# Performance work log

Hardware: AMD Instinct MI355X
Metric: run time of the kernel (lower is better)

The kernel has to match this reference:

```python
import jax, jax.numpy as jnp
import numpy as np

M, N, K, C, H = 100000, 8192, 32, 256, 8
DH = C // H
FF = 512
R = (15, 15, 7)  # 2*MAXRANGE-1 per axis for MAXRANGE=[8,8,4]


def _layer_norm(x, g, b, eps=1e-5):
    mu = jnp.mean(x, axis=-1, keepdims=True)
    xc = x - mu
    var = jnp.mean(xc * xc, axis=-1, keepdims=True)
    return xc * jax.lax.rsqrt(var + eps) * g + b


def setup_inputs() -> dict:
    key = jax.random.key(0)
    ks = iter(jax.random.split(key, 40))
    d = {}
    d['voxel_features'] = jax.random.normal(next(ks), (M, C), jnp.float32)
    d['query_coords'] = jax.random.normal(next(ks), (N, 3), jnp.float32)
    d['query_indices'] = jax.random.randint(next(ks), (N,), 0, M)
    d['gather_indices'] = jax.random.randint(next(ks), (N, K), 0, M)
    d['gather_mask'] = jax.random.randint(next(ks), (N, K), 0, 2).astype(bool)
    d['rel_x'] = jax.random.randint(next(ks), (N, K), 0, R[0])
    d['rel_y'] = jax.random.randint(next(ks), (N, K), 0, R[1])
    d['rel_z'] = jax.random.randint(next(ks), (N, K), 0, R[2])
    s = 0.02
    # pos_proj: Conv1d(3, C, 1) == linear on coords
    d['w_pos'] = jax.random.normal(next(ks), (3, C), jnp.float32) * s
    d['b_pos'] = jnp.zeros((C,), jnp.float32)
    for nm in ['q', 'k', 'v', 'proj']:
        d['w_' + nm] = jax.random.normal(next(ks), (C, C), jnp.float32) * (C ** -0.5)
        d['b_' + nm] = jnp.zeros((C,), jnp.float32)
    d['ln1_g'] = jnp.ones((C,), jnp.float32); d['ln1_b'] = jnp.zeros((C,), jnp.float32)
    d['ln2_g'] = jnp.ones((C,), jnp.float32); d['ln2_b'] = jnp.zeros((C,), jnp.float32)
    d['w_ff1'] = jax.random.normal(next(ks), (C, FF), jnp.float32) * (C ** -0.5)
    d['b_ff1'] = jnp.zeros((FF,), jnp.float32)
    d['w_ff2'] = jax.random.normal(next(ks), (FF, C), jnp.float32) * (FF ** -0.5)
    d['b_ff2'] = jnp.zeros((C,), jnp.float32)
    # per-axis relative position tables: [H, DH, 2W-1] for q-side and k-side
    for m in ['q', 'k']:
        for ax, r in zip(['x', 'y', 'z'], R):
            d[f'pos_{m}{ax}'] = jax.random.normal(next(ks), (H, DH, r), jnp.float32) * s
    return d


def reference(voxel_features, query_coords, query_indices, gather_indices, gather_mask,
              rel_x, rel_y, rel_z,
              w_pos, b_pos, w_q, b_q, w_k, b_k, w_v, b_v, w_proj, b_proj,
              ln1_g, ln1_b, ln2_g, ln2_b, w_ff1, b_ff1, w_ff2, b_ff2,
              pos_qx, pos_qy, pos_qz, pos_kx, pos_ky, pos_kz):
    x = _layer_norm(voxel_features, ln1_g, ln1_b)           # [M, C] pre-norm
    # gather window centers (queries) + positional projection of coords
    q_in = x[query_indices] + jax.nn.relu(query_coords @ w_pos + b_pos)  # [N, C]
    kv_in = x[gather_indices]                                # [N, K, C]
    kv_in = jnp.where(gather_mask[..., None], 0.0, kv_in)
    q = (q_in @ w_q + b_q).reshape(N, H, DH)
    k = (kv_in @ w_k + b_k).reshape(N, K, H, DH)
    v = (kv_in @ w_v + b_v).reshape(N, K, H, DH)
    logits = jnp.einsum('nhd,nkhd->nhk', q, k) * (DH ** -0.5)  # [N, H, K]
    # query-side per-axis relative position bias: contract q with table, gather at rel idx
    for pos, rel in ((pos_qx, rel_x), (pos_qy, rel_y), (pos_qz, rel_z)):
        qp = jnp.einsum('nhd,hdr->nhr', q, pos)              # [N, H, R]
        logits = logits + jnp.take_along_axis(qp, rel[:, None, :], axis=2)
    # key-side per-axis relative position bias
    for pos, rel in ((pos_kx, rel_x), (pos_ky, rel_y), (pos_kz, rel_z)):
        kp = jnp.einsum('nkhd,hdr->nkhr', k, pos)            # [N, K, H, R]
        bias = jnp.take_along_axis(kp, rel[:, :, None, None], axis=3)[..., 0]  # [N, K, H]
        logits = logits + bias.transpose(0, 2, 1)
    logits = jnp.where(gather_mask[:, None, :], -1e9, logits)
    attn = jax.nn.softmax(logits, axis=-1)
    out = jnp.einsum('nhk,nkhd->nhd', attn, v).reshape(N, C) @ w_proj + b_proj
    act = voxel_features[query_indices] + out                # residual (pre-norm block)
    h = jax.nn.relu(_layer_norm(act, ln2_g, ln2_b) @ w_ff1 + b_ff1) @ w_ff2 + b_ff2
    return act + h                                           # [N, C]
```

## Files before the change

kernel.cpp:

```cpp
#include <hip/hip_runtime.h>
#include <hip/hip_bf16.h>
#include <math.h>

#define MV   100000
#define NQ   8192
#define KN   32
#define CH   256
#define NH   8
#define DHD  32
#define FFD  512
#define NG   (NQ*KN)
#define QPW  37
#define QPN  (NH*QPW)
#define QPL  320
#define ASTR 40

typedef __bf16 bf16x8 __attribute__((ext_vector_type(8)));
typedef float  f32x4  __attribute__((ext_vector_type(4)));

__device__ __forceinline__ float bf2f(unsigned short u) {
    return __uint_as_float(((unsigned int)u) << 16);
}
__device__ __forceinline__ unsigned short f2bf(float f) {
    unsigned int x = __float_as_uint(f);
    unsigned int r = x + 0x7FFFu + ((x >> 16) & 1u);
    return (unsigned short)(r >> 16);
}
__device__ __forceinline__ void glds16(const unsigned short* g, unsigned short* l) {
    __builtin_amdgcn_global_load_lds(
        (const __attribute__((address_space(1))) void*)g,
        (__attribute__((address_space(3))) void*)l, 16, 0, 0);
}

__global__ __launch_bounds__(256) void k_detect_mask(const unsigned char* __restrict__ raw,
                                                     int* __restrict__ flags) {
    __shared__ int any;
    if (threadIdx.x == 0) any = 0;
    __syncthreads();
    const uint4* p = (const uint4*)raw;
    int i = blockIdx.x * 256 + threadIdx.x;
    uint4 v = p[i];
    if ((v.x | v.y | v.z | v.w) & 0xFFFFFF00u) any = 1;
    __syncthreads();
    if (threadIdx.x == 0) flags[blockIdx.x] = any;
}

__global__ __launch_bounds__(256) void k_prep(const float* __restrict__ w_k,
                                              const float* __restrict__ w_v,
                                              const float* __restrict__ w_ff1,
                                              const float* __restrict__ w_ff2,
                                              const float* __restrict__ w_proj,
                                              const float* __restrict__ w_q,
                                              const float* __restrict__ b_k,
                                              const float* __restrict__ b_v,
                                              const float* __restrict__ pos_qx,
                                              const float* __restrict__ pos_qy,
                                              const float* __restrict__ pos_qz,
                                              const void* __restrict__ mask_raw,
                                              const int* __restrict__ gidx,
                                              const int* __restrict__ flags,
                                              unsigned short* __restrict__ w_kv_t,
                                              unsigned short* __restrict__ w1_t,
                                              unsigned short* __restrict__ w2_t,
                                              unsigned short* __restrict__ wp_t,
                                              unsigned short* __restrict__ wq_t,
                                              unsigned short* __restrict__ wqp_t,
                                              float* __restrict__ bkv,
                                              float* __restrict__ zbias,
                                              int* __restrict__ mask_i,
                                              unsigned char* __restrict__ touched) {
    __shared__ int bl;
    if (threadIdx.x == 0) {
        int a = 0;
        #pragma unroll 8
        for (int i = 0; i < 64; i++) a |= flags[i];
        bl = a;
    }
    __syncthreads();
    int byteLayout = bl;
    int idx = blockIdx.x * 256 + threadIdx.x;
    if (blockIdx.x == 0 && threadIdx.x < 512)
        bkv[threadIdx.x] = (threadIdx.x < 256) ? b_k[threadIdx.x]
                                               : b_v[threadIdx.x - 256];
    if (idx < QPL) zbias[idx] = 0.f;
    if (idx < NG) {
        int mv = byteLayout ? (int)((const unsigned char*)mask_raw)[idx]
                            : ((const int*)mask_raw)[idx];
        mask_i[idx] = (mv != 0) ? 1 : 0;
        if (mv == 0) touched[gidx[idx]] = 1;
    }
    if (idx < 512 * 256) {
        int col = idx >> 8, j = idx & 255;
        float v = (col < 256) ? w_k[j * 256 + col] : w_v[j * 256 + (col - 256)];
        w_kv_t[idx] = f2bf(v);
    }
    if (idx < 512 * 256) {
        int n = idx >> 8, k = idx & 255;
        w1_t[idx] = f2bf(w_ff1[k * FFD + n]);
    }
    if (idx < 256 * 512) {
        int n = idx >> 9, k = idx & 511;
        w2_t[idx] = f2bf(w_ff2[k * CH + n]);
    }
    if (idx < 256 * 256) {
        int n = idx >> 8, k = idx & 255;
        wp_t[idx] = f2bf(w_proj[k * CH + n]);
        wq_t[idx] = f2bf(w_q[k * CH + n]);
    }
    if (idx < QPL * 256) {
        int col = idx >> 8, k = idx & 255;
        float v = 0.f;
        if (col < QPN) {
            int h = col / QPW, r = col % QPW;
            int h2 = k >> 5, d = k & 31;
            if (h2 == h) {
                if (r < 15)      v = pos_qx[(h * DHD + d) * 15 + r];
                else if (r < 30) v = pos_qy[(h * DHD + d) * 15 + (r - 15)];
                else             v = pos_qz[(h * DHD + d) * 7  + (r - 30)];
            }
        }
        wqp_t[idx] = f2bf(v);
    }
}

__global__ __launch_bounds__(256) void k_posc(const float* __restrict__ pos_kx,
                                              const float* __restrict__ pos_ky,
                                              const float* __restrict__ pos_kz,
                                              float* __restrict__ comb) {
    int idx = blockIdx.x * 256 + threadIdx.x;
    if (idx >= 8 * 15 * 15 * 7 * 32) return;
    int d = idx & 31, r = idx >> 5;
    int rz = r % 7;  r /= 7;
    int ry = r % 15; r /= 15;
    int rx = r % 15; int h = r / 15;
    comb[idx] = pos_kx[(h * DHD + d) * 15 + rx]
              + pos_ky[(h * DHD + d) * 15 + ry]
              + pos_kz[(h * DHD + d) * 7  + rz];
}

__global__ __launch_bounds__(256) void k_ln(const float* __restrict__ x,
                                            const float* __restrict__ g,
                                            const float* __restrict__ b,
                                            unsigned short* __restrict__ o,
                                            int nrows) {
    int wid = threadIdx.x >> 6, lane = threadIdx.x & 63;
    int row = blockIdx.x * 4 + wid;
    if (row >= nrows) return;
    const float4 v = *(const float4*)(x + (size_t)row * CH + lane * 4);
    float s  = v.x + v.y + v.z + v.w;
    float sq = v.x * v.x + v.y * v.y + v.z * v.z + v.w * v.w;
    #pragma unroll
    for (int off = 1; off < 64; off <<= 1) {
        s  += __shfl_xor(s,  off);
        sq += __shfl_xor(sq, off);
    }
    float mu  = s * (1.f / CH);
    float var = sq * (1.f / CH) - mu * mu;
    float rs  = rsqrtf(var + 1e-5f);
    float4 gv = *(const float4*)(g + lane * 4);
    float4 bv = *(const float4*)(b + lane * 4);
    ushort4 ov;
    ov.x = f2bf((v.x - mu) * rs * gv.x + bv.x);
    ov.y = f2bf((v.y - mu) * rs * gv.y + bv.y);
    ov.z = f2bf((v.z - mu) * rs * gv.z + bv.z);
    ov.w = f2bf((v.w - mu) * rs * gv.w + bv.w);
    *(ushort4*)(o + (size_t)row * CH + lane * 4) = ov;
}

__global__ __launch_bounds__(256) void k_qin(const unsigned short* __restrict__ ln_x,
                                             const float* __restrict__ coords,
                                             const int* __restrict__ qidx,
                                             const float* __restrict__ w_pos,
                                             const float* __restrict__ b_pos,
                                             unsigned short* __restrict__ qin) {
    int c = threadIdx.x;
    int nb = blockIdx.x * 8;
    float wp0 = w_pos[c], wp1 = w_pos[CH + c], wp2 = w_pos[2 * CH + c], bp = b_pos[c];
    #pragma unroll
    for (int qq = 0; qq < 8; qq++) {
        int n = nb + qq;
        float p = bp + coords[n * 3] * wp0 + coords[n * 3 + 1] * wp1 + coords[n * 3 + 2] * wp2;
        p = fmaxf(p, 0.f);
        int qi = qidx[n];
        qin[(size_t)n * CH + c] = f2bf(bf2f(ln_x[(size_t)qi * CH + c]) + p);
    }
}

__global__ __launch_bounds__(256) void k_kv(const unsigned short* __restrict__ ln_x,
                                            const unsigned short* __restrict__ w_kv_t,
                                            const float* __restrict__ bkv,
                                            const unsigned char* __restrict__ touched,
                                            unsigned short* __restrict__ kv) {
    __shared__ __align__(16) unsigned short As[8 * 4096];
    __shared__ __align__(16) unsigned short Bs[4096];
    const int tid = threadIdx.x;
    const int w = tid >> 6, l = tid & 63;
    const int wr = w >> 1, wc = w & 1;
    const int rowbase = blockIdx.x * 128;
    const int sr = l >> 2, sq = l & 3;
    const int ml = l & 15, qd = l >> 4;

    int ra0 = rowbase + w * 16 + sr;
    int ra1 = rowbase + 64 + w * 16 + sr;
    int ok0 = (ra0 < MV) && touched[ra0 < MV ? ra0 : 0];
    int ok1 = (ra1 < MV) && touched[ra1 < MV ? ra1 : 0];
    const unsigned short* pa0 = ln_x + (size_t)(ok0 ? ra0 : rowbase) * CH + sq * 8;
    const unsigned short* pa1 = ln_x + (size_t)(ok1 ? ra1 : rowbase) * CH + sq * 8;
    unsigned short* lA0 = As + w * 512;
    unsigned short* lA1 = As + 2048 + w * 512;
    unsigned short* lB0 = Bs + w * 512;
    unsigned short* lB1 = Bs + 2048 + w * 512;

    #pragma unroll
    for (int c = 0; c < 8; c++) {
        glds16(pa0 + c * 32, lA0 + c * 4096);
        glds16(pa1 + c * 32, lA1 + c * 4096);
    }

    for (int ct = 0; ct < 4; ct++) {
        const int col0 = ct * 128;
        const unsigned short* pb0 = w_kv_t + (size_t)(col0 + w * 16 + sr) * CH + sq * 8;
        const unsigned short* pb1 = w_kv_t + (size_t)(col0 + 64 + w * 16 + sr) * CH + sq * 8;
        f32x4 acc[4][4];
        #pragma unroll
        for (int mt = 0; mt < 4; mt++)
            #pragma unroll
            for (int nt = 0; nt < 4; nt++)
                acc[mt][nt] = (f32x4){0.f, 0.f, 0.f, 0.f};

        for (int c = 0; c < 8; c++) {
            __syncthreads();
            glds16(pb0 + c * 32, lB0);
            glds16(pb1 + c * 32, lB1);
            __syncthreads();
            bf16x8 af[4], bf[4];
            const unsigned short* Ac = As + c * 4096;
            #pragma unroll
            for (int mt = 0; mt < 4; mt++)
                af[mt] = *(const bf16x8*)(Ac + (wr * 64 + mt * 16 + ml) * 32 + qd * 8);
            #pragma unroll
            for (int nt = 0; nt < 4; nt++)
                bf[nt] = *(const bf16x8*)(Bs + (wc * 64 + nt * 16 + ml) * 32 + qd * 8);
            #pragma unroll
            for (int mt = 0; mt < 4; mt++)
                #pragma unroll
                for (int nt = 0; nt < 4; nt++)
                    acc[mt][nt] = __builtin_amdgcn_mfma_f32_16x16x32_bf16(af[mt], bf[nt], acc[mt][nt], 0, 0, 0);
        }

        float bb[4];
        #pragma unroll
        for (int nt = 0; nt < 4; nt++)
            bb[nt] = bkv[col0 + wc * 64 + nt * 16 + ml];
        #pragma unroll
        for (int mt = 0; mt < 4; mt++) {
            __syncthreads();
            #pragma unroll
            for (int nt = 0; nt < 4; nt++) {
                int lcol = wc * 64 + nt * 16 + ml;
                #pragma unroll
                for (int i = 0; i < 4; i++)
                    Bs[wr * 2048 + (qd * 4 + i) * 128 + lcol] = f2bf(acc[mt][nt][i] + bb[nt]);
            }
            __syncthreads();
            int rl = tid >> 4, cc = (tid & 15) * 8;
            int g0 = rowbase + mt * 16 + rl;
            int g1 = rowbase + 64 + mt * 16 + rl;
            if (g0 < MV && touched[g0])
                *(uint4*)(kv + (size_t)g0 * 512 + col0 + cc) = *(const uint4*)(Bs + rl * 128 + cc);
            if (g1 < MV && touched[g1])
                *(uint4*)(kv + (size_t)g1 * 512 + col0 + cc) = *(const uint4*)(Bs + 2048 + rl * 128 + cc);
        }
    }
}

template <int KD, int EPI, int LDO>
__global__ __launch_bounds__(256) void k_mm(const unsigned short* __restrict__ A,
                                            const unsigned short* __restrict__ Bt_g,
                                            const float* __restrict__ bias,
                                            const float* __restrict__ res,
                                            const int* __restrict__ qidx,
                                            unsigned short* __restrict__ out_bf,
                                            float* __restrict__ out_f) {
    __shared__ __align__(16) unsigned short As[128 * ASTR];
    __shared__ __align__(16) unsigned short Bs[64 * ASTR];
    int tid = threadIdx.x;
    int w = tid >> 6, l = tid & 63;
    int rowbase = blockIdx.y * 128;
    int col0 = blockIdx.x * 64;
    int r0 = tid >> 2, qt = tid & 3;
    const unsigned short* a0p = A + (size_t)(rowbase + r0) * KD + qt * 8;
    const unsigned short* a1p = A + (size_t)(rowbase + 64 + r0) * KD + qt * 8;

    f32x4 acc[2][4];
    #pragma unroll
    for (int mt = 0; mt < 2; mt++)
        #pragma unroll
        for (int nt = 0; nt < 4; nt++)
            acc[mt][nt] = (f32x4){0.f, 0.f, 0.f, 0.f};

    const int ml = l & 15, qd = l >> 4;
    for (int kk = 0; kk < KD; kk += 32) {
        __syncthreads();
        uint4 v0 = *(const uint4*)(a0p + kk);
        uint4 v1 = *(const uint4*)(a1p + kk);
        *(uint4*)(As + r0 * ASTR + qt * 8)        = v0;
        *(uint4*)(As + (64 + r0) * ASTR + qt * 8) = v1;
        {
            uint4 bv = *(const uint4*)(Bt_g + (size_t)(col0 + r0) * KD + kk + qt * 8);
            *(uint4*)(Bs + r0 * ASTR + qt * 8) = bv;
        }
        __syncthreads();
        bf16x8 a0 = *(const bf16x8*)(As + (w * 32 + ml) * ASTR + qd * 8);
        bf16x8 a1 = *(const bf16x8*)(As + (w * 32 + 16 + ml) * ASTR + qd * 8);
        #pragma unroll
        for (int nt = 0; nt < 4; nt++) {
            bf16x8 bb = *(const bf16x8*)(Bs + (nt * 16 + ml) * ASTR + qd * 8);
            acc[0][nt] = __builtin_amdgcn_mfma_f32_16x16x32_bf16(a0, bb, acc[0][nt], 0, 0, 0);
            acc[1][nt] = __builtin_amdgcn_mfma_f32_16x16x32_bf16(a1, bb, acc[1][nt], 0, 0, 0);
        }
    }

    #pragma unroll
    for (int nt = 0; nt < 4; nt++) {
        int col = col0 + nt * 16 + ml;
        float bv = bias[col];
        #pragma unroll
        for (int mt = 0; mt < 2; mt++) {
            int rl = w * 32 + mt * 16 + qd * 4;
            #pragma unroll
            for (int i = 0; i < 4; i++) {
                int row = rowbase + rl + i;
                float v = acc[mt][nt][i] + bv;
                if (EPI == 0) {
                    out_bf[(size_t)row * LDO + col] = f2bf(fmaxf(v, 0.f));
                } else if (EPI == 1) {
                    out_f[(size_t)row * CH + col] = v + res[(size_t)row * CH + col];
                } else if (EPI == 2) {
                    int qi = qidx[row];
                    out_f[(size_t)row * CH + col] = v + res[(size_t)qi * CH + col];
                } else if (EPI == 3) {
                    out_f[(size_t)row * CH + col] = v;
                    out_bf[(size_t)row * CH + col] = f2bf(v);
                } else {
                    out_f[(size_t)row * LDO + col] = v;
                }
            }
        }
    }
}

__global__ __launch_bounds__(256) void k_attn2(const float* __restrict__ qbuf,
                                               const float* __restrict__ qp,
                                               const unsigned short* __restrict__ kvmat,
                                               const int* __restrict__ gidx,
                                               const int* __restrict__ mask_i,
                                               const int* __restrict__ rel_x,
                                               const int* __restrict__ rel_y,
                                               const int* __restrict__ rel_z,
                                               const float* __restrict__ comb,
                                               const float* __restrict__ b_v,
                                               unsigned short* __restrict__ attnln) {
    __shared__ float q_s[1024];
    __shared__ float qp_s[4 * QPL];
    __shared__ float attn_s[4 * 256];
    __shared__ int mask_s[4 * 32];
    int tid = threadIdx.x;
    int qb = blockIdx.x * 4;
    for (int i = tid; i < 1024; i += 256) q_s[i] = qbuf[(size_t)qb * CH + i];
    for (int i = tid; i < 4 * QPL; i += 256) qp_s[i] = qp[(size_t)qb * QPL + i];
    if (tid < 128) mask_s[tid] = mask_i[qb * 32 + tid];
    __syncthreads();
    int h = tid >> 5, k = tid & 31;
    const float scale = 0.17677669529663687f;
    for (int qq = 0; qq < 4; qq++) {
        int n = qb + qq;
        int gi = n * KN + k;
        int mk = mask_s[qq * 32 + k];
        float lg = -1e9f;
        if (!mk) {
            int rx = rel_x[gi], ry = rel_y[gi], rz = rel_z[gi];
            int g = gidx[gi];
            const uint4* kp = (const uint4*)(kvmat + (size_t)g * 512 + h * DHD);
            float kv[32];
            #pragma unroll
            for (int j = 0; j < 4; j++) {
                uint4 u = kp[j];
                kv[j * 8 + 0] = bf2f((unsigned short)(u.x & 0xFFFF));
                kv[j * 8 + 1] = bf2f((unsigned short)(u.x >> 16));
                kv[j * 8 + 2] = bf2f((unsigned short)(u.y & 0xFFFF));
                kv[j * 8 + 3] = bf2f((unsigned short)(u.y >> 16));
                kv[j * 8 + 4] = bf2f((unsigned short)(u.z & 0xFFFF));
                kv[j * 8 + 5] = bf2f((unsigned short)(u.z >> 16));
                kv[j * 8 + 6] = bf2f((unsigned short)(u.w & 0xFFFF));
                kv[j * 8 + 7] = bf2f((unsigned short)(u.w >> 16));
            }
            const float* cp = comb + ((((h * 15 + rx) * 15 + ry) * 7 + rz) << 5);
            float s1 = 0.f, s2 = 0.f;
            const float* qrow = q_s + qq * CH + h * DHD;
            #pragma unroll
            for (int d = 0; d < 32; d++) {
                s1 += kv[d] * qrow[d];
                s2 += kv[d] * cp[d];
            }
            lg = s1 * scale + s2
               + qp_s[qq * QPL + h * QPW + rx]
               + qp_s[qq * QPL + h * QPW + 15 + ry]
               + qp_s[qq * QPL + h * QPW + 30 + rz];
        }
        float mx = lg;
        #pragma unroll
        for (int off = 1; off <= 16; off <<= 1) mx = fmaxf(mx, __shfl_xor(mx, off));
        float e = mk ? 0.f : __expf(lg - mx);
        float sm = e;
        #pragma unroll
        for (int off = 1; off <= 16; off <<= 1) sm += __shfl_xor(sm, off);
        attn_s[qq * 256 + tid] = (sm > 0.f) ? e / sm : 0.f;
    }
    __syncthreads();

    int w = tid >> 6, l = tid & 63;
    int n = qb + w;
    int hh = l >> 3;
    float a0 = 0.f, a1 = 0.f, a2 = 0.f, a3 = 0.f;
    int nm = 0;
    for (int kk = 0; kk < KN; kk++) {
        if (mask_s[w * 32 + kk]) continue;
        nm++;
        int g = gidx[n * 32 + kk];
        ushort4 v4 = *(const ushort4*)(kvmat + (size_t)g * 512 + 256 + l * 4);
        float av = attn_s[w * 256 + hh * 32 + kk];
        a0 += av * bf2f(v4.x);
        a1 += av * bf2f(v4.y);
        a2 += av * bf2f(v4.z);
        a3 += av * bf2f(v4.w);
    }
    int col = l * 4;
    if (nm == 0) {
        a0 = b_v[col]; a1 = b_v[col + 1]; a2 = b_v[col + 2]; a3 = b_v[col + 3];
    }
    ushort4 o;
    o.x = f2bf(a0); o.y = f2bf(a1); o.z = f2bf(a2); o.w = f2bf(a3);
    *(ushort4*)(attnln + (size_t)n * CH + col) = o;
}

extern "C" void kernel_launch(void* const* d_in, const int* in_sizes, int n_in,
                              void* d_out, int out_size, void* d_ws, size_t ws_size,
                              hipStream_t stream) {
    (void)in_sizes; (void)n_in; (void)out_size; (void)ws_size;
    const float* vox    = (const float*)d_in[0];
    const float* coords = (const float*)d_in[1];
    const int*   qidx   = (const int*)d_in[2];
    const int*   gidx   = (const int*)d_in[3];
    const void*  mraw   = d_in[4];
    const int*   rel_x  = (const int*)d_in[5];
    const int*   rel_y  = (const int*)d_in[6];
    const int*   rel_z  = (const int*)d_in[7];
    const float* w_pos  = (const float*)d_in[8];
    const float* b_pos  = (const float*)d_in[9];
    const float* w_q    = (const float*)d_in[10];
    const float* b_q    = (const float*)d_in[11];
    const float* w_k    = (const float*)d_in[12];
    const float* b_k    = (const float*)d_in[13];
    const float* w_v    = (const float*)d_in[14];
    const float* b_v    = (const float*)d_in[15];
    const float* w_proj = (const float*)d_in[16];
    const float* b_proj = (const float*)d_in[17];
    const float* ln1_g  = (const float*)d_in[18];
    const float* ln1_b  = (const float*)d_in[19];
    const float* ln2_g  = (const float*)d_in[20];
    const float* ln2_b  = (const float*)d_in[21];
    const float* w_ff1  = (const float*)d_in[22];
    const float* b_ff1  = (const float*)d_in[23];
    const float* w_ff2  = (const float*)d_in[24];
    const float* b_ff2  = (const float*)d_in[25];
    const float* pos_qx = (const float*)d_in[26];
    const float* pos_qy = (const float*)d_in[27];
    const float* pos_qz = (const float*)d_in[28];
    const float* pos_kx = (const float*)d_in[29];
    const float* pos_ky = (const float*)d_in[30];
    const float* pos_kz = (const float*)d_in[31];

    char* p = (char*)d_ws;
    auto take = [&](size_t n) { char* r = p; p += (n + 255) & ~(size_t)255; return r; };
    unsigned short* ln_x    = (unsigned short*)take((size_t)MV * CH * 2);
    unsigned short* w_kv_t  = (unsigned short*)take((size_t)512 * 256 * 2);
    unsigned short* w1_t    = (unsigned short*)take((size_t)512 * 256 * 2);
    unsigned short* w2_t    = (unsigned short*)take((size_t)256 * 512 * 2);
    unsigned short* wp_t    = (unsigned short*)take((size_t)256 * 256 * 2);
    unsigned short* wq_t    = (unsigned short*)take((size_t)256 * 256 * 2);
    unsigned short* wqp_t   = (unsigned short*)take((size_t)QPL * 256 * 2);
    float*          bkv     = (float*)take(512 * 4);
    float*          zbias   = (float*)take(QPL * 4);
    int*            flags   = (int*)take(64 * 4);
    int*            mask_i  = (int*)take((size_t)NG * 4);
    unsigned char*  touched = (unsigned char*)take(MV);
    float*          comb    = (float*)take((size_t)8 * 15 * 15 * 7 * 32 * 4);
    unsigned short* qin     = (unsigned short*)take((size_t)NQ * CH * 2);
    float*          qbuf    = (float*)take((size_t)NQ * CH * 4);
    unsigned short* qbf     = (unsigned short*)take((size_t)NQ * CH * 2);
    float*          qp      = (float*)take((size_t)NQ * QPL * 4);
    unsigned short* kvmat   = (unsigned short*)take((size_t)MV * 512 * 2);
    unsigned short* attnln  = (unsigned short*)take((size_t)NQ * CH * 2);
    float*          actbuf  = (float*)take((size_t)NQ * CH * 4);
    unsigned short* actln   = (unsigned short*)take((size_t)NQ * CH * 2);
    unsigned short* hbuf    = (unsigned short*)take((size_t)NQ * FFD * 2);

    hipMemsetAsync(touched, 0, MV, stream);
    hipLaunchKernelGGL(k_detect_mask, dim3(64), dim3(256), 0, stream,
                       (const unsigned char*)mraw, flags);
    hipLaunchKernelGGL(k_prep, dim3(NG / 256), dim3(256), 0, stream,
                       w_k, w_v, w_ff1, w_ff2, w_proj, w_q, b_k, b_v,
                       pos_qx, pos_qy, pos_qz, mraw, gidx, flags,
                       w_kv_t, w1_t, w2_t, wp_t, wq_t, wqp_t, bkv, zbias,
                       mask_i, touched);
    hipLaunchKernelGGL(k_posc, dim3((8 * 15 * 15 * 7 * 32 + 255) / 256), dim3(256), 0, stream,
                       pos_kx, pos_ky, pos_kz, comb);
    hipLaunchKernelGGL(k_ln, dim3(MV / 4 + 1), dim3(256), 0, stream,
                       vox, ln1_g, ln1_b, ln_x, MV);
    hipLaunchKernelGGL(k_qin, dim3(NQ / 8), dim3(256), 0, stream,
                       ln_x, coords, qidx, w_pos, b_pos, qin);
    hipLaunchKernelGGL(k_kv, dim3((MV + 127) / 128), dim3(256), 0, stream,
                       ln_x, w_kv_t, bkv, touched, kvmat);
    hipLaunchKernelGGL(HIP_KERNEL_NAME(k_mm<256, 3, CH>), dim3(4, NQ / 128), dim3(256), 0, stream,
                       qin, wq_t, b_q, (const float*)nullptr, (const int*)nullptr,
                       qbf, qbuf);
    hipLaunchKernelGGL(HIP_KERNEL_NAME(k_mm<256, 4, QPL>), dim3(QPL / 64, NQ / 128), dim3(256), 0, stream,
                       qbf, wqp_t, zbias, (const float*)nullptr, (const int*)nullptr,
                       (unsigned short*)nullptr, qp);
    hipLaunchKernelGGL(k_attn2, dim3(NQ / 4), dim3(256), 0, stream,
                       qbuf, qp, kvmat, gidx, mask_i, rel_x, rel_y, rel_z,
                       comb, b_v, attnln);
    hipLaunchKernelGGL(HIP_KERNEL_NAME(k_mm<256, 2, CH>), dim3(4, NQ / 128), dim3(256), 0, stream,
                       attnln, wp_t, b_proj, vox, qidx,
                       (unsigned short*)nullptr, actbuf);
    hipLaunchKernelGGL(k_ln, dim3(NQ / 4), dim3(256), 0, stream,
                       actbuf, ln2_g, ln2_b, actln, NQ);
    hipLaunchKernelGGL(HIP_KERNEL_NAME(k_mm<256, 0, FFD>), dim3(8, NQ / 128), dim3(256), 0, stream,
                       actln, w1_t, b_ff1, (const float*)nullptr, (const int*)nullptr,
                       hbuf, (float*)nullptr);
    hipLaunchKernelGGL(HIP_KERNEL_NAME(k_mm<512, 1, CH>), dim3(4, NQ / 128), dim3(256), 0, stream,
                       hbuf, w2_t, b_ff2, actbuf, (const int*)nullptr,
                       (unsigned short*)nullptr, (float*)d_out);
}
```

Baseline: 416.8 us.

## Stage gathered K/V rows in LDS with coalesced loads, two queries per block

The attention kernel now gathers each neighbor's K and V rows into padded shared memory using fully coalesced 16-byte loads per row, issued up front with the loads in flight together. Previously each thread fetched K slices scattered by head and re-read V rows per query. Blocks handle two queries instead of four, doubling the grid, and the V accumulation is split across two half-warps per query with a reduction through shared memory. This costs more LDS per block (about 34KB), which may limit occupancy, plus extra barriers.

```diff
diff --git a/kernel.cpp b/kernel.cpp
--- a/kernel.cpp
+++ b/kernel.cpp
@@ -14,6 +14,7 @@
 #define QPN  (NH*QPW)
 #define QPL  320
 #define ASTR 40
+#define KSTR 264
 
 typedef __bf16 bf16x8 __attribute__((ext_vector_type(8)));
 typedef float  f32x4  __attribute__((ext_vector_type(4)));
@@ -350,7 +351,7 @@
     }
 }
 
-__global__ __launch_bounds__(256) void k_attn2(const float* __restrict__ qbuf,
+__global__ __launch_bounds__(256) void k_attn3(const float* __restrict__ qbuf,
                                                const float* __restrict__ qp,
                                                const unsigned short* __restrict__ kvmat,
                                                const int* __restrict__ gidx,
@@ -361,31 +362,54 @@
                                                const float* __restrict__ comb,
                                                const float* __restrict__ b_v,
                                                unsigned short* __restrict__ attnln) {
-    __shared__ float q_s[1024];
-    __shared__ float qp_s[4 * QPL];
-    __shared__ float attn_s[4 * 256];
-    __shared__ int mask_s[4 * 32];
+    __shared__ float q_s[2 * 256];
+    __shared__ float qp_s[2 * QPL];
+    __shared__ float attn_s[2 * 256];
+    __shared__ int   mask_s[64];
+    __shared__ int   gidx_s[64];
+    __shared__ __align__(16) unsigned short ks[64 * KSTR];
+
     int tid = threadIdx.x;
-    int qb = blockIdx.x * 4;
-    for (int i = tid; i < 1024; i += 256) q_s[i] = qbuf[(size_t)qb * CH + i];
-    for (int i = tid; i < 4 * QPL; i += 256) qp_s[i] = qp[(size_t)qb * QPL + i];
-    if (tid < 128) mask_s[tid] = mask_i[qb * 32 + tid];
-    __syncthreads();
+    int qb = blockIdx.x * 2;
+    for (int i = tid; i < 512; i += 256) q_s[i] = qbuf[(size_t)qb * CH + i];
+    for (int i = tid; i < 2 * QPL; i += 256) qp_s[i] = qp[(size_t)qb * QPL + i];
+    if (tid < 64) {
+        mask_s[tid] = mask_i[qb * 32 + tid];
+        gidx_s[tid] = gidx[qb * 32 + tid];
+    }
+    __syncthreads();
+
+    const int srow = tid >> 5;
+    const int schk = tid & 31;
+    uint4 kreg[8];
+    #pragma unroll
+    for (int j = 0; j < 8; j++) {
+        int r = j * 8 + srow;
+        uint4 v = {0u, 0u, 0u, 0u};
+        if (!mask_s[r])
+            v = *(const uint4*)(kvmat + (size_t)gidx_s[r] * 512 + schk * 8);
+        kreg[j] = v;
+    }
+    #pragma unroll
+    for (int j = 0; j < 8; j++)
+        *(uint4*)(ks + (j * 8 + srow) * KSTR + schk * 8) = kreg[j];
+    __syncthreads();
+
     int h = tid >> 5, k = tid & 31;
     const float scale = 0.17677669529663687f;
-    for (int qq = 0; qq < 4; qq++) {
+    for (int qq = 0; qq < 2; qq++) {
         int n = qb + qq;
         int gi = n * KN + k;
-        int mk = mask_s[qq * 32 + k];
+        int r = qq * 32 + k;
+        int mk = mask_s[r];
         float lg = -1e9f;
         if (!mk) {
             int rx = rel_x[gi], ry = rel_y[gi], rz = rel_z[gi];
-            int g = gidx[gi];
-            const uint4* kp = (const uint4*)(kvmat + (size_t)g * 512 + h * DHD);
+            const unsigned short* kp = ks + r * KSTR + h * 32;
             float kv[32];
             #pragma unroll
             for (int j = 0; j < 4; j++) {
-                uint4 u = kp[j];
+                uint4 u = *(const uint4*)(kp + j * 8);
                 kv[j * 8 + 0] = bf2f((unsigned short)(u.x & 0xFFFF));
                 kv[j * 8 + 1] = bf2f((unsigned short)(u.x >> 16));
                 kv[j * 8 + 2] = bf2f((unsigned short)(u.y & 0xFFFF));
@@ -417,31 +441,55 @@
         for (int off = 1; off <= 16; off <<= 1) sm += __shfl_xor(sm, off);
         attn_s[qq * 256 + tid] = (sm > 0.f) ? e / sm : 0.f;
     }
+
+    #pragma unroll
+    for (int j = 0; j < 8; j++) {
+        int r = j * 8 + srow;
+        uint4 v = {0u, 0u, 0u, 0u};
+        if (!mask_s[r])
+            v = *(const uint4*)(kvmat + (size_t)gidx_s[r] * 512 + 256 + schk * 8);
+        kreg[j] = v;
+    }
+    __syncthreads();
+    #pragma unroll
+    for (int j = 0; j < 8; j++)
+        *(uint4*)(ks + (j * 8 + srow) * KSTR + schk * 8) = kreg[j];
     __syncthreads();
 
     int w = tid >> 6, l = tid & 63;
-    int n = qb + w;
+    int q2 = w >> 1, kh = w & 1;
     int hh = l >> 3;
     float a0 = 0.f, a1 = 0.f, a2 = 0.f, a3 = 0.f;
-    int nm = 0;
-    for (int kk = 0; kk < KN; kk++) {
-        if (mask_s[w * 32 + kk]) continue;
-        nm++;
-        int g = gidx[n * 32 + kk];
-        ushort4 v4 = *(const ushort4*)(kvmat + (size_t)g * 512 + 256 + l * 4);
-        float av = attn_s[w * 256 + hh * 32 + kk];
+    #pragma unroll
+    for (int i = 0; i < 16; i++) {
+        int kk = kh * 16 + i;
+        int r = q2 * 32 + kk;
+        float av = attn_s[q2 * 256 + hh * 32 + kk];
+        ushort4 v4 = *(const ushort4*)(ks + r * KSTR + l * 4);
         a0 += av * bf2f(v4.x);
         a1 += av * bf2f(v4.y);
         a2 += av * bf2f(v4.z);
         a3 += av * bf2f(v4.w);
     }
-    int col = l * 4;
-    if (nm == 0) {
-        a0 = b_v[col]; a1 = b_v[col + 1]; a2 = b_v[col + 2]; a3 = b_v[col + 3];
-    }
-    ushort4 o;
-    o.x = f2bf(a0); o.y = f2bf(a1); o.z = f2bf(a2); o.w = f2bf(a3);
-    *(ushort4*)(attnln + (size_t)n * CH + col) = o;
+    if (kh == 1) {
+        float4 pv = {a0, a1, a2, a3};
+        *(float4*)(qp_s + q2 * 256 + l * 4) = pv;
+    }
+    __syncthreads();
+    if (kh == 0) {
+        float4 pv = *(const float4*)(qp_s + q2 * 256 + l * 4);
+        a0 += pv.x; a1 += pv.y; a2 += pv.z; a3 += pv.w;
+        int nm = 0;
+        #pragma unroll
+        for (int kk = 0; kk < 32; kk++) nm += 1 - mask_s[q2 * 32 + kk];
+        int col = l * 4;
+        if (nm == 0) {
+            a0 = b_v[col]; a1 = b_v[col + 1]; a2 = b_v[col + 2]; a3 = b_v[col + 3];
+        }
+        ushort4 o;
+        o.x = f2bf(a0); o.y = f2bf(a1); o.z = f2bf(a2); o.w = f2bf(a3);
+        *(ushort4*)(attnln + (size_t)(qb + q2) * CH + col) = o;
+    }
 }
 
 extern "C" void kernel_launch(void* const* d_in, const int* in_sizes, int n_in,
@@ -528,7 +576,7 @@
     hipLaunchKernelGGL(HIP_KERNEL_NAME(k_mm<256, 4, QPL>), dim3(QPL / 64, NQ / 128), dim3(256), 0, stream,
                        qbf, wqp_t, zbias, (const float*)nullptr, (const int*)nullptr,
                        (unsigned short*)nullptr, qp);
-    hipLaunchKernelGGL(k_attn2, dim3(NQ / 4), dim3(256), 0, stream,
+    hipLaunchKernelGGL(k_attn3, dim3(NQ / 2), dim3(256), 0, stream,
                        qbuf, qp, kvmat, gidx, mask_i, rel_x, rel_y, rel_z,
                        comb, b_v, attnln);
     hipLaunchKernelGGL(HIP_KERNEL_NAME(k_mm<256, 2, CH>), dim3(4, NQ / 128), dim3(256), 0, stream,
```

After: 401.8 us. 3.6% less time.
